# Optimization experiments

Measured on AMD Instinct MI355X. Metric: run time of the kernel, lower is better.

The kernel has to match this reference:

```python
import jax, jax.numpy as jnp
import numpy as np

BINS = 100
NORMALIZE = False
SIGMA = 1.0
B, N = 128, 512
EDGE_P = 0.02  # edge probability -> avg degree ~10


def _make_adj(key):
    u = jax.random.uniform(key, (B, N, N))
    a = (u < EDGE_P).astype(jnp.float32)
    up = jnp.triu(a, 1)
    return up + jnp.swapaxes(up, -1, -2)  # symmetric, zero diagonal


def setup_inputs() -> dict:
    key = jax.random.key(0)
    k1, k2 = jax.random.split(key)
    return {"adj_1": _make_adj(k1), "adj_2": _make_adj(k2)}


def _clustering_hist(adj):
    # adj: [B, N, N] binary symmetric, zero diag
    deg = adj.sum(-1)                                   # [B, N]
    a2 = jnp.matmul(adj, adj)                           # [B, N, N]
    tri2 = jnp.einsum('bij,bji->bi', a2, adj)           # diag(A^3) = 2 * triangles
    denom = deg * (deg - 1.0)
    # nx.clustering: c_i = 2*T_i / (k_i*(k_i-1)) = diag(A^3)_i / (k_i*(k_i-1)); 0 if k_i < 2
    c = jnp.where(denom > 0, tri2 / jnp.maximum(denom, 1.0), 0.0)  # [B, N] in [0,1]
    # histogram over [0,1] with BINS bins; value 1.0 falls in last bin (torch.histogram semantics)
    idx = jnp.clip((c * BINS).astype(jnp.int32), 0, BINS - 1)
    hist = jax.vmap(lambda ix: jnp.zeros((BINS,), jnp.float32).at[ix].add(1.0))(idx)
    if NORMALIZE:
        hist = hist * (BINS / N)  # density: count / (n_samples * bin_width)
    return hist  # [B, BINS]


def _rbf_mmd(x, y, sigma):
    # biased MMD^2 estimate with RBF kernel
    def kmat(a, b):
        sq = (a * a).sum(-1)[:, None] + (b * b).sum(-1)[None, :] - 2.0 * (a @ b.T)
        return jnp.exp(-jnp.maximum(sq, 0.0) / (2.0 * sigma * sigma))
    return kmat(x, x).mean() + kmat(y, y).mean() - 2.0 * kmat(x, y).mean()


def reference(adj_1, adj_2):
    h1 = _clustering_hist(adj_1)
    h2 = _clustering_hist(adj_2)
    return _rbf_mmd(h1, h2, SIGMA)
```

## Files before the change

kernel.cpp:

```cpp
#include <hip/hip_runtime.h>
#include <stdint.h>

#define BATCH 128
#define NN 512
#define BINS 100
#define WORDS 8
#define WPAD 9
#define ECAP 6144

__device__ __forceinline__ unsigned long long spread4(unsigned long long x) {
    x = (x | (x << 24)) & 0x000000ff000000ffull;
    x = (x | (x << 12)) & 0x000f000f000f000full;
    x = (x | (x <<  6)) & 0x0303030303030303ull;
    x = (x | (x <<  3)) & 0x1111111111111111ull;
    return x;
}

__global__ __launch_bounds__(1024) void k_cluster_hist(
    const float* __restrict__ adj1, const float* __restrict__ adj2,
    float* __restrict__ hist )
{
    __shared__ unsigned long long bits[NN][WPAD];
    __shared__ unsigned int edges[ECAP];
    __shared__ int tri2[NN];
    __shared__ int histI[BINS];
    __shared__ int ecnt;

    const int gb = blockIdx.x;
    const float* __restrict__ gp =
        (gb < BATCH ? adj1 : adj2) + (size_t)(gb & (BATCH - 1)) * NN * NN;

    const int tid  = threadIdx.x;
    const int lane = tid & 63;
    const int wave = tid >> 6;

    if (tid < BINS) histI[tid] = 0;
    if (tid < NN)   tri2[tid]  = 0;
    if (tid == 0)   ecnt = 0;

    for (int r = wave; r < NN; r += 16) {
        const int br = r >> 6;
        const int nb = 8 - br;
        const int c0 = br << 6;
        const int rr = r & 63;
        const int Lmin = (rr < 3) ? 0 : ((rr + 1) >> 2);
        float4 v = make_float4(0.f, 0.f, 0.f, 0.f);
        if (lane < 16 * nb && (lane >= 16 || lane >= Lmin))
            v = *(const float4*)(gp + (size_t)r * NN + c0 + 4 * lane);
        unsigned long long b0 = __ballot(v.x != 0.0f);
        unsigned long long b1 = __ballot(v.y != 0.0f);
        unsigned long long b2 = __ballot(v.z != 0.0f);
        unsigned long long b3 = __ballot(v.w != 0.0f);
        if (lane < nb) {
            const int sh = 16 * lane;
            unsigned long long w =
                (spread4((b0 >> sh) & 0xFFFFull) << 0) |
                (spread4((b1 >> sh) & 0xFFFFull) << 1) |
                (spread4((b2 >> sh) & 0xFFFFull) << 2) |
                (spread4((b3 >> sh) & 0xFFFFull) << 3);
            bits[r][br + lane] = w;
        }
    }
    __syncthreads();

    for (int p = wave; p < 36; p += 16) {
        int bi, bj;
        if (p < 28) {
            bi = 1;
            while (bi * (bi + 1) / 2 <= p) ++bi;
            bj = p - bi * (bi - 1) / 2;
        } else {
            bi = p - 28; bj = bi;
        }
        unsigned long long x = bits[(bj << 6) + lane][bi];
        unsigned long long t = x;
        const unsigned long long M[6] = {
            0x5555555555555555ull, 0x3333333333333333ull,
            0x0f0f0f0f0f0f0f0full, 0x00ff00ff00ff00ffull,
            0x0000ffff0000ffffull, 0x00000000ffffffffull };
        #pragma unroll
        for (int s = 0; s < 6; ++s) {
            const int k = 1 << s;
            unsigned long long y = __shfl_xor((long long)t, k, 64);
            if ((lane & k) == 0) t = (t &  M[s]) | ((y &  M[s]) << k);
            else                 t = (t & ~M[s]) | ((y & ~M[s]) >> k);
        }
        if (p < 28) bits[(bi << 6) + lane][bj] = t;
        else        bits[(bi << 6) + lane][bi] = x | t;
    }
    __syncthreads();

    for (int p = tid; p < NN * WORDS; p += 1024) {
        int r = p >> 3;
        int m = p & 7;
        unsigned long long w = bits[r][m];
        int base = m << 6;
        int sh = r - base + 1;
        unsigned long long wm =
            (sh <= 0) ? w : (sh >= 64 ? 0ull : (w & (~0ull << sh)));
        int cnt = __popcll(wm);

        int x = cnt;
        #pragma unroll
        for (int off = 1; off < 64; off <<= 1) {
            int y = __shfl_up(x, off, 64);
            if (lane >= off) x += y;
        }
        int excl = x - cnt;
        int bs = 0;
        if (lane == 63) bs = atomicAdd(&ecnt, x);
        bs = __shfl(bs, 63, 64);

        int idx = bs + excl;
        while (wm) {
            int L = __builtin_ctzll(wm);
            wm &= wm - 1;
            int j = base + L;
            if (idx < ECAP) edges[idx] = ((unsigned)r << 10) | (unsigned)j;
            ++idx;
        }
    }
    __syncthreads();

    const int ne = ecnt < ECAP ? ecnt : ECAP;
    for (int e = tid; e < ne; e += 1024) {
        unsigned ed = edges[e];
        int i = ed >> 10;
        int j = ed & 1023;
        int acc = 0;
        #pragma unroll
        for (int w = 0; w < WORDS; ++w)
            acc += __popcll(bits[i][w] & bits[j][w]);
        atomicAdd(&tri2[i], acc);
        atomicAdd(&tri2[j], acc);
    }
    __syncthreads();

    if (tid < NN) {
        int deg = 0;
        #pragma unroll
        for (int w = 0; w < WORDS; ++w) deg += __popcll(bits[tid][w]);
        float t2    = (float)tri2[tid];
        float degf  = (float)deg;
        float denom = degf * (degf - 1.0f);
        float c = denom > 0.0f ? t2 / denom : 0.0f;
        int idx = (int)(c * 100.0f);
        idx = idx < 0 ? 0 : (idx > BINS - 1 ? BINS - 1 : idx);
        atomicAdd(&histI[idx], 1);
    }
    __syncthreads();

    if (tid < BINS) hist[(size_t)gb * BINS + tid] = (float)histI[tid];
}

__global__ __launch_bounds__(256) void k_mmd_partial(
    const float* __restrict__ hist, float* __restrict__ partials)
{
    int p = blockIdx.x * 256 + threadIdx.x;
    int t   = p >> 14;
    int rem = p & 16383;
    int i = rem >> 7;
    int j = rem & 127;
    const float4* x4;
    const float4* y4;
    float w;
    if (t == 0)      { x4 = (const float4*)(hist + (size_t)i * BINS);           y4 = (const float4*)(hist + (size_t)j * BINS);           w =  1.0f; }
    else if (t == 1) { x4 = (const float4*)(hist + (size_t)(BATCH + i) * BINS); y4 = (const float4*)(hist + (size_t)(BATCH + j) * BINS); w =  1.0f; }
    else             { x4 = (const float4*)(hist + (size_t)i * BINS);           y4 = (const float4*)(hist + (size_t)(BATCH + j) * BINS); w = -2.0f; }
    float sq = 0.0f;
    #pragma unroll
    for (int k = 0; k < BINS / 4; ++k) {
        float4 a = x4[k];
        float4 b = y4[k];
        float d0 = a.x - b.x, d1 = a.y - b.y, d2 = a.z - b.z, d3 = a.w - b.w;
        sq += d0 * d0 + d1 * d1 + d2 * d2 + d3 * d3;
    }
    float local = w * expf(-0.5f * sq);

    __shared__ float red[256];
    red[threadIdx.x] = local;
    __syncthreads();
    for (int s = 128; s >= 1; s >>= 1) {
        if (threadIdx.x < s) red[threadIdx.x] += red[threadIdx.x + s];
        __syncthreads();
    }
    if (threadIdx.x == 0) partials[blockIdx.x] = red[0];
}

__global__ __launch_bounds__(64) void k_mmd_final(
    const float* __restrict__ partials, float* __restrict__ out, int nparts)
{
    int lane = threadIdx.x;
    float v = 0.0f;
    for (int p = lane; p < nparts; p += 64) v += partials[p];
    #pragma unroll
    for (int off = 32; off >= 1; off >>= 1) v += __shfl_xor(v, off, 64);
    if (lane == 0) out[0] = v * (1.0f / (float)(BATCH * BATCH));
}

extern "C" void kernel_launch(void* const* d_in, const int* in_sizes, int n_in,
                              void* d_out, int out_size, void* d_ws, size_t ws_size,
                              hipStream_t stream) {
    const float* a1 = (const float*)d_in[0];
    const float* a2 = (const float*)d_in[1];
    float* out = (float*)d_out;

    const size_t hist_bytes = (size_t)2 * BATCH * BINS * 4;
    float* hist     = (float*)d_ws;
    float* partials = (float*)((char*)d_ws + hist_bytes);

    hipLaunchKernelGGL(k_cluster_hist, dim3(2 * BATCH), dim3(1024), 0, stream,
                       a1, a2, hist);
    hipLaunchKernelGGL(k_mmd_partial, dim3(192), dim3(256), 0, stream,
                       hist, partials);
    hipLaunchKernelGGL(k_mmd_final, dim3(1), dim3(64), 0, stream,
                       partials, out, 192);
}
```

Baseline: 258.0 us.

## Split adjacency bit-packing into a separate massively parallel pack kernel

Moves the float-to-bitmask packing of the adjacency matrices out of the per-graph kernel into its own kernel, where each wave packs half a row, giving 12288 blocks instead of 256. The upper-triangle reads now cover the diagonal 64x64 blocks fully, so the diagonal transpose-and-OR step is dropped. The triangle kernel then loads the packed bits from a global workspace buffer. This is meant to spread the memory-bound read of 256 MB of floats across the whole GPU instead of 256 blocks. The cost is an extra kernel launch and a round trip of 8 MB of packed words through global memory.

```diff
diff --git a/kernel.cpp b/kernel.cpp
--- a/kernel.cpp
+++ b/kernel.cpp
@@ -16,8 +16,46 @@
     return x;
 }
 
-__global__ __launch_bounds__(1024) void k_cluster_hist(
+
+#define PACK_WAVES (2 * BATCH * 768)
+#define PACK_BLOCKS (PACK_WAVES / 16)
+
+__global__ __launch_bounds__(1024) void k_pack(
     const float* __restrict__ adj1, const float* __restrict__ adj2,
+    unsigned long long* __restrict__ ub )
+{
+    const int wv   = blockIdx.x * 16 + (threadIdx.x >> 6);
+    const int lane = threadIdx.x & 63;
+    const int g    = wv / 768;
+    const int rem  = wv - g * 768;
+    const int h    = rem < NN ? 1 : 0;
+    const int r    = h ? rem : rem - NN;
+    const int br   = r >> 6;
+    const int ws   = h ? (br > 4 ? br - 4 : 0) : br;
+
+    const float* __restrict__ gp =
+        (g < BATCH ? adj1 : adj2) + (size_t)(g & (BATCH - 1)) * NN * NN;
+
+    float4 v = make_float4(0.f, 0.f, 0.f, 0.f);
+    if (lane >= 16 * ws)
+        v = *(const float4*)(gp + (size_t)r * NN + (h << 8) + 4 * lane);
+    unsigned long long b0 = __ballot(v.x != 0.0f);
+    unsigned long long b1 = __ballot(v.y != 0.0f);
+    unsigned long long b2 = __ballot(v.z != 0.0f);
+    unsigned long long b3 = __ballot(v.w != 0.0f);
+    if (lane >= ws && lane < 4) {
+        const int sh = 16 * lane;
+        unsigned long long w =
+            (spread4((b0 >> sh) & 0xFFFFull) << 0) |
+            (spread4((b1 >> sh) & 0xFFFFull) << 1) |
+            (spread4((b2 >> sh) & 0xFFFFull) << 2) |
+            (spread4((b3 >> sh) & 0xFFFFull) << 3);
+        ub[((size_t)(g * NN + r) << 3) + (h << 2) + lane] = w;
+    }
+}
+
+__global__ __launch_bounds__(1024) void k_tri_hist(
+    const unsigned long long* __restrict__ ub,
     float* __restrict__ hist )
 {
     __shared__ unsigned long long bits[NN][WPAD];
@@ -26,10 +64,7 @@
     __shared__ int histI[BINS];
     __shared__ int ecnt;
 
-    const int gb = blockIdx.x;
-    const float* __restrict__ gp =
-        (gb < BATCH ? adj1 : adj2) + (size_t)(gb & (BATCH - 1)) * NN * NN;
-
+    const int gb   = blockIdx.x;
     const int tid  = threadIdx.x;
     const int lane = tid & 63;
     const int wave = tid >> 6;
@@ -38,42 +73,16 @@
     if (tid < NN)   tri2[tid]  = 0;
     if (tid == 0)   ecnt = 0;
 
-    for (int r = wave; r < NN; r += 16) {
-        const int br = r >> 6;
-        const int nb = 8 - br;
-        const int c0 = br << 6;
-        const int rr = r & 63;
-        const int Lmin = (rr < 3) ? 0 : ((rr + 1) >> 2);
-        float4 v = make_float4(0.f, 0.f, 0.f, 0.f);
-        if (lane < 16 * nb && (lane >= 16 || lane >= Lmin))
-            v = *(const float4*)(gp + (size_t)r * NN + c0 + 4 * lane);
-        unsigned long long b0 = __ballot(v.x != 0.0f);
-        unsigned long long b1 = __ballot(v.y != 0.0f);
-        unsigned long long b2 = __ballot(v.z != 0.0f);
-        unsigned long long b3 = __ballot(v.w != 0.0f);
-        if (lane < nb) {
-            const int sh = 16 * lane;
-            unsigned long long w =
-                (spread4((b0 >> sh) & 0xFFFFull) << 0) |
-                (spread4((b1 >> sh) & 0xFFFFull) << 1) |
-                (spread4((b2 >> sh) & 0xFFFFull) << 2) |
-                (spread4((b3 >> sh) & 0xFFFFull) << 3);
-            bits[r][br + lane] = w;
-        }
-    }
-    __syncthreads();
-
-    for (int p = wave; p < 36; p += 16) {
-        int bi, bj;
-        if (p < 28) {
-            bi = 1;
-            while (bi * (bi + 1) / 2 <= p) ++bi;
-            bj = p - bi * (bi - 1) / 2;
-        } else {
-            bi = p - 28; bj = bi;
-        }
-        unsigned long long x = bits[(bj << 6) + lane][bi];
-        unsigned long long t = x;
+    const unsigned long long* __restrict__ gsrc = ub + ((size_t)gb << 12);
+    for (int p = tid; p < NN * WORDS; p += 1024)
+        bits[p >> 3][p & 7] = gsrc[p];
+    __syncthreads();
+
+    for (int p = wave; p < 28; p += 16) {
+        int bi = 1;
+        while (bi * (bi + 1) / 2 <= p) ++bi;
+        int bj = p - bi * (bi - 1) / 2;
+        unsigned long long t = bits[(bj << 6) + lane][bi];
         const unsigned long long M[6] = {
             0x5555555555555555ull, 0x3333333333333333ull,
             0x0f0f0f0f0f0f0f0full, 0x00ff00ff00ff00ffull,
@@ -85,8 +94,7 @@
             if ((lane & k) == 0) t = (t &  M[s]) | ((y &  M[s]) << k);
             else                 t = (t & ~M[s]) | ((y & ~M[s]) >> k);
         }
-        if (p < 28) bits[(bi << 6) + lane][bj] = t;
-        else        bits[(bi << 6) + lane][bi] = x | t;
+        bits[(bi << 6) + lane][bj] = t;
     }
     __syncthreads();
 
@@ -208,9 +216,13 @@
     const size_t hist_bytes = (size_t)2 * BATCH * BINS * 4;
     float* hist     = (float*)d_ws;
     float* partials = (float*)((char*)d_ws + hist_bytes);
-
-    hipLaunchKernelGGL(k_cluster_hist, dim3(2 * BATCH), dim3(1024), 0, stream,
-                       a1, a2, hist);
+    unsigned long long* ub =
+        (unsigned long long*)((char*)d_ws + 103424);
+
+    hipLaunchKernelGGL(k_pack, dim3(PACK_BLOCKS), dim3(1024), 0, stream,
+                       a1, a2, ub);
+    hipLaunchKernelGGL(k_tri_hist, dim3(2 * BATCH), dim3(1024), 0, stream,
+                       ub, hist);
     hipLaunchKernelGGL(k_mmd_partial, dim3(192), dim3(256), 0, stream,
                        hist, partials);
     hipLaunchKernelGGL(k_mmd_final, dim3(1), dim3(64), 0, stream,
```

After: 273.4 us. +6.0%, slower.
